# Performance work log

Measured on AMD Instinct MI355X. Metric: run time of the kernel, lower is better.

The kernel has to match this reference:

```python
import jax, jax.numpy as jnp
import numpy as np

B, N, K, DIM = 2, 20000, 16, 256


def _mlp(x, W, b):
    # torch nn.Linear: x @ W.T + b, then LeakyReLU(0.1)
    return jax.nn.leaky_relu(x @ W.T + b, negative_slope=0.1)


def _lfa(features, geom, idx, W, b):
    # features: [B, N, C]; geom: [B, N, K, 4]; idx: [B, N, K]
    t = _mlp(geom, W, b)                                  # [B, N, K, d_lfa]
    fn = jax.vmap(lambda f, i: f[i])(features, idx)       # gather neighbors: [B, N, K, C]
    # mean over K of concat == concat of means (faithful, avoids big concat)
    return jnp.concatenate([t.mean(axis=2), fn.mean(axis=2)], axis=-1)


def _linear_init(key, out_f, in_f):
    k1, k2 = jax.random.split(key)
    bound = 1.0 / np.sqrt(in_f)
    W = jax.random.uniform(k1, (out_f, in_f), jnp.float32, -bound, bound)
    b = jax.random.uniform(k2, (out_f,), jnp.float32, -bound, bound)
    return W, b


def setup_inputs() -> dict:
    key = jax.random.key(0)
    ks = jax.random.split(key, 8)
    W_init, b_init = _linear_init(ks[0], DIM // 4, DIM)
    W_l1, b_l1 = _linear_init(ks[1], DIM // 4, 4)
    W_l2, b_l2 = _linear_init(ks[2], DIM // 2, 4)
    W_fin, b_fin = _linear_init(ks[3], DIM, DIM)
    W_id, b_id = _linear_init(ks[4], DIM, DIM)
    return {
        "input_tensor": jax.random.normal(ks[5], (B, N, DIM), jnp.float32),
        "geometric_features": jax.random.normal(ks[6], (B, N, K, 4), jnp.float32),
        "neighbor_indices": jax.random.randint(ks[7], (B, N, K), 0, N, jnp.int64 if jax.config.jax_enable_x64 else jnp.int32),
        "W_init": W_init, "b_init": b_init,
        "W_l1": W_l1, "b_l1": b_l1,
        "W_l2": W_l2, "b_l2": b_l2,
        "W_fin": W_fin, "b_fin": b_fin,
        "W_id": W_id, "b_id": b_id,
    }


def reference(input_tensor, geometric_features, neighbor_indices,
              W_init, b_init, W_l1, b_l1, W_l2, b_l2,
              W_fin, b_fin, W_id, b_id):
    residual = input_tensor
    x = _mlp(input_tensor, W_init, b_init)                       # [B, N, dim/4]
    x = _lfa(x, geometric_features, neighbor_indices, W_l1, b_l1)  # [B, N, dim/2]
    x = _lfa(x, geometric_features, neighbor_indices, W_l2, b_l2)  # [B, N, dim]
    x = _mlp(x, W_fin, b_fin)
    return x + _mlp(residual, W_id, b_id)
```

## Files before the change

### kernel.cpp

```cpp
#include <hip/hip_runtime.h>
#include <hip/hip_bf16.h>

#define BN   40000
#define NPTS 20000
#define KNN  16
#define DIM  256

typedef __attribute__((ext_vector_type(8))) short bf16x8;
typedef __attribute__((ext_vector_type(4))) float f32x4;

__device__ __forceinline__ float lrelu(float v) { return v > 0.f ? v : 0.1f * v; }
__device__ __forceinline__ float bs2f(short s) {
    union { unsigned u; float f; } c; c.u = ((unsigned)(unsigned short)s) << 16;
    return c.f;
}
__device__ __forceinline__ short f2bs(float f) {
    __hip_bfloat16 h = __float2bfloat16(f);
    return *reinterpret_cast<short*>(&h);
}
__device__ __forceinline__ bf16x8 ldf32_bf16x8(const float* p) {
    const float4 a = ((const float4*)p)[0];
    const float4 b = ((const float4*)p)[1];
    bf16x8 r;
    r[0]=f2bs(a.x); r[1]=f2bs(a.y); r[2]=f2bs(a.z); r[3]=f2bs(a.w);
    r[4]=f2bs(b.x); r[5]=f2bs(b.y); r[6]=f2bs(b.z); r[7]=f2bs(b.w);
    return r;
}

__device__ __forceinline__ void dma16(const void* g, void* l) {
    __builtin_amdgcn_global_load_lds(
        (const __attribute__((address_space(1))) unsigned int*)g,
        (__attribute__((address_space(3))) unsigned int*)l, 16, 0, 0);
}

__global__ void __launch_bounds__(256) geom_kernel(
    const float* __restrict__ geom,
    const float* __restrict__ W1, const float* __restrict__ B1,
    const float* __restrict__ W2, const float* __restrict__ B2,
    const int* __restrict__ idxw, int* __restrict__ flag,
    const float* __restrict__ Wf, const float* __restrict__ Wi,
    const float* __restrict__ Wn,
    short* __restrict__ Wt, short* __restrict__ Wnt,
    __hip_bfloat16* __restrict__ x2,
    __hip_bfloat16* __restrict__ x3)
{
    if (blockIdx.x >= 3751) {
        int t = (blockIdx.x - 3751) * 256 + threadIdx.x;
        if (t < 32768) {
            int mat = (t >> 14) & 1;
            int tt  = t & 16383;
            float4 v = mat ? ((const float4*)Wi)[tt] : ((const float4*)Wf)[tt];
            int n  = tt >> 6;
            int k  = (tt & 63) * 4;
            int kk = k >> 5, q = (k >> 3) & 3, j = k & 7;
            short4 o; o.x=f2bs(v.x); o.y=f2bs(v.y); o.z=f2bs(v.z); o.w=f2bs(v.w);
            *(short4*)(Wt + ((size_t)((kk*2 + mat)*4 + q))*2048 + n*8 + j) = o;
        } else {
            int tt = t - 32768;
            float4 v = ((const float4*)Wn)[tt];
            int n  = tt >> 6;
            int k  = (tt & 63) * 4;
            int kk = k >> 5, q = (k >> 3) & 3, j = k & 7;
            short4 o; o.x=f2bs(v.x); o.y=f2bs(v.y); o.z=f2bs(v.z); o.w=f2bs(v.w);
            *(short4*)(Wnt + ((size_t)((kk*4 + q)*64 + n))*8 + j) = o;
        }
        return;
    }
    if (blockIdx.x == 3750) {
        __shared__ int red[256];
        int t = threadIdx.x;
        int v = 0;
#pragma unroll
        for (int it = 0; it < 64; ++it)
            v |= idxw[2 * (t + it * 256) + 1];
        red[t] = v;
        __syncthreads();
        for (int s = 128; s > 0; s >>= 1) {
            if (t < s) red[t] |= red[t + s];
            __syncthreads();
        }
        if (t == 0) *flag = (red[0] != 0) ? 1 : 0;
        return;
    }
    int tid = blockIdx.x * 256 + threadIdx.x;
    int p  = tid / 24;
    int cg = tid - p * 24;
    const float4* g = (const float4*)(geom + (size_t)p * (KNN * 4));
    const float4* Wp; const float* Bp; int c0;
    if (cg < 8) { c0 = cg * 8;       Wp = (const float4*)W1; Bp = B1; }
    else        { c0 = (cg - 8) * 8; Wp = (const float4*)W2; Bp = B2; }
    float4 w[8]; float bb[8];
#pragma unroll
    for (int j = 0; j < 8; ++j) { w[j] = Wp[c0 + j]; bb[j] = Bp[c0 + j]; }
    float acc[8];
#pragma unroll
    for (int j = 0; j < 8; ++j) acc[j] = 0.f;
#pragma unroll
    for (int k = 0; k < KNN; ++k) {
        float4 gv = g[k];
#pragma unroll
        for (int j = 0; j < 8; ++j)
            acc[j] += lrelu(bb[j] + gv.x*w[j].x + gv.y*w[j].y + gv.z*w[j].z + gv.w*w[j].w);
    }
    const float s = 1.f/16.f;
    short* dst = (cg < 8) ? ((short*)x2 + (size_t)p*128 + c0)
                          : ((short*)x3 + (size_t)p*256 + c0);
    bf16x8 o;
#pragma unroll
    for (int j = 0; j < 8; ++j) o[j] = f2bs(acc[j] * s);
    *(bf16x8*)dst = o;
}

__global__ void __launch_bounds__(256) mlp_init_mfma(
    const float* __restrict__ X,
    const short* __restrict__ Wnt,
    const float* __restrict__ bias,
    __hip_bfloat16* __restrict__ Y)
{
    __shared__ short wbuf[16384];
    int t = threadIdx.x;
    int wave = t >> 6, lane = t & 63;
    int r = lane & 15, q = lane >> 4;
    {
        const char* W8 = (const char*)Wnt;
        char* L8 = (char*)wbuf;
#pragma unroll
        for (int rd = 0; rd < 8; ++rd) {
            int off = (wave * 8 + rd) * 1024 + lane * 16;
            dma16(W8 + off, L8 + off);
        }
    }
    int m0 = blockIdx.x * 64 + wave * 16;
    const float* Xs = X + (size_t)(m0 + r) * DIM + q * 8;
    bf16x8 a[8];
#pragma unroll
    for (int kk = 0; kk < 8; ++kk) a[kk] = ldf32_bf16x8(Xs + kk * 32);
    __syncthreads();

    f32x4 acc[4];
#pragma unroll
    for (int nt = 0; nt < 4; ++nt) acc[nt] = (f32x4){0.f,0.f,0.f,0.f};
#pragma unroll
    for (int kk = 0; kk < 8; ++kk) {
#pragma unroll
        for (int nt = 0; nt < 4; ++nt) {
            bf16x8 b = *(const bf16x8*)&wbuf[((kk*4 + q)*64 + nt*16 + r) * 8];
            acc[nt] = __builtin_amdgcn_mfma_f32_16x16x32_bf16(a[kk], b, acc[nt], 0, 0, 0);
        }
    }
#pragma unroll
    for (int nt = 0; nt < 4; ++nt) {
        int col = nt * 16 + r;
        float bv = bias[col];
#pragma unroll
        for (int i = 0; i < 4; ++i) {
            float v = lrelu(acc[nt][i] + bv);
            Y[(size_t)(m0 + q*4 + i) * 64 + col] = __float2bfloat16(v);
        }
    }
}

__global__ void __launch_bounds__(256) gather1_kernel(
    const int* __restrict__ idxw, const int* __restrict__ flag,
    const __hip_bfloat16* __restrict__ x1,
    __hip_bfloat16* __restrict__ x2)
{
    int t = blockIdx.x * 256 + threadIdx.x;
    int p = t >> 3, j = t & 7;
    int lane = threadIdx.x & 63;
    int dual = (*flag == 0) ? 2 : 1;
    int base = (p >= NPTS) ? NPTS : 0;
    int i0 = idxw[((size_t)p * 16 + 2*j)     * dual];
    int i1 = idxw[((size_t)p * 16 + 2*j + 1) * dual];
    int g8 = lane & 56;
    float acc[8];
#pragma unroll
    for (int i = 0; i < 8; ++i) acc[i] = 0.f;
#pragma unroll
    for (int k = 0; k < 8; ++k) {
        int rA = base + __shfl(i0, g8 + k, 64);
        int rB = base + __shfl(i1, g8 + k, 64);
        bf16x8 vA = *(const bf16x8*)((const short*)x1 + (size_t)rA * 64 + j * 8);
        bf16x8 vB = *(const bf16x8*)((const short*)x1 + (size_t)rB * 64 + j * 8);
#pragma unroll
        for (int i = 0; i < 8; ++i) acc[i] += bs2f(vA[i]) + bs2f(vB[i]);
    }
    bf16x8 o;
#pragma unroll
    for (int i = 0; i < 8; ++i) o[i] = f2bs(acc[i] * (1.f/16.f));
    *(bf16x8*)((short*)x2 + (size_t)p * 128 + 64 + j * 8) = o;
}

__global__ void __launch_bounds__(256) gather2_kernel(
    const int* __restrict__ idxw, const int* __restrict__ flag,
    const __hip_bfloat16* __restrict__ x2,
    __hip_bfloat16* __restrict__ x3)
{
    int t = blockIdx.x * 256 + threadIdx.x;
    int p = t >> 4, j = t & 15;
    int lane = threadIdx.x & 63;
    int dual = (*flag == 0) ? 2 : 1;
    int base = (p >= NPTS) ? NPTS : 0;
    int myi = idxw[((size_t)p * 16 + j) * dual];
    int g16 = lane & 48;
    float acc[8];
#pragma unroll
    for (int i = 0; i < 8; ++i) acc[i] = 0.f;
#pragma unroll
    for (int k = 0; k < KNN; ++k) {
        int row = base + __shfl(myi, g16 + k, 64);
        bf16x8 v = *(const bf16x8*)((const short*)x2 + (size_t)row * 128 + j * 8);
#pragma unroll
        for (int i = 0; i < 8; ++i) acc[i] += bs2f(v[i]);
    }
    bf16x8 o;
#pragma unroll
    for (int i = 0; i < 8; ++i) o[i] = f2bs(acc[i] * (1.f/16.f));
    *(bf16x8*)((short*)x3 + (size_t)p * 256 + 128 + j * 8) = o;
}

__global__ void __launch_bounds__(512, 2) final_mfma(
    const __hip_bfloat16* __restrict__ X3,
    const float* __restrict__ RES,
    const short* __restrict__ Wt,
    const float* __restrict__ Bf,
    const float* __restrict__ Bi,
    float* __restrict__ OUT)
{
    __shared__ short lw[65536];
    const int t    = threadIdx.x;
    const int wave = t >> 6, lane = t & 63;
    const int r = lane & 15, q = lane >> 4;
    const int rg = wave >> 1, cg = wave & 1;
    const int ch = blockIdx.x & 1;
    const int p0 = (blockIdx.x >> 1) * 320;

    {
        const char* WtB = (const char*)Wt;
        char* L = (char*)lw;
#pragma unroll
        for (int i = 0; i < 16; ++i) {
            int c = wave * 8 + (i >> 1);
            int d = i & 1;
            int mat = c >> 5, kk = (c >> 2) & 7, qq = c & 3;
            int src_sh = ((kk * 2 + mat) * 4 + qq) * 2048 + ch * 1024;
            dma16(WtB + (size_t)src_sh * 2 + d * 1024 + lane * 16,
                  L + (c * 2 + d) * 1024 + lane * 16);
        }
    }
    const int cb = ch * 128 + cg * 64;
    float bfv[4], biv[4];
#pragma unroll
    for (int nt = 0; nt < 4; ++nt) {
        bfv[nt] = Bf[cb + nt * 16 + r];
        biv[nt] = Bi[cb + nt * 16 + r];
    }
    __syncthreads();

    const short* bpf = lw + q * 1024 + (cg * 64 + r) * 8;
    const short* bpi = bpf + 32768;

#pragma unroll
    for (int tt = 0; tt < 5; ++tt) {
        const int row = p0 + tt * 64 + rg * 16 + r;
        const short* x3r = (const short*)X3 + (size_t)row * DIM + q * 8;
        const float* rsr = RES + (size_t)row * DIM + q * 8;

        bf16x8 a1[8];
        float4 rw[16];
#pragma unroll
        for (int kk = 0; kk < 8; ++kk) {
            rw[2*kk]   = ((const float4*)rsr)[kk * 8];
            rw[2*kk+1] = ((const float4*)rsr)[kk * 8 + 1];
            a1[kk] = *(const bf16x8*)(x3r + kk * 32);
        }

        f32x4 acc1[4], acc2[4];
#pragma unroll
        for (int nt = 0; nt < 4; ++nt) {
            acc1[nt] = (f32x4){0.f,0.f,0.f,0.f};
            acc2[nt] = (f32x4){0.f,0.f,0.f,0.f};
        }
#pragma unroll
        for (int kk = 0; kk < 8; ++kk) {
            bf16x8 a2;
            {
                const float4 lo = rw[2*kk], hi = rw[2*kk+1];
                a2[0]=f2bs(lo.x); a2[1]=f2bs(lo.y); a2[2]=f2bs(lo.z); a2[3]=f2bs(lo.w);
                a2[4]=f2bs(hi.x); a2[5]=f2bs(hi.y); a2[6]=f2bs(hi.z); a2[7]=f2bs(hi.w);
            }
#pragma unroll
            for (int nt = 0; nt < 4; ++nt) {
                bf16x8 b1 = *(const bf16x8*)(bpf + kk * 4096 + nt * 128);
                bf16x8 b2 = *(const bf16x8*)(bpi + kk * 4096 + nt * 128);
                acc1[nt] = __builtin_amdgcn_mfma_f32_16x16x32_bf16(a1[kk], b1, acc1[nt], 0, 0, 0);
                acc2[nt] = __builtin_amdgcn_mfma_f32_16x16x32_bf16(a2,    b2, acc2[nt], 0, 0, 0);
            }
        }
#pragma unroll
        for (int nt = 0; nt < 4; ++nt) {
            const int col = cb + nt * 16 + r;
#pragma unroll
            for (int i = 0; i < 4; ++i) {
                float v = lrelu(acc1[nt][i] + bfv[nt]) + lrelu(acc2[nt][i] + biv[nt]);
                OUT[(size_t)(p0 + tt * 64 + rg * 16 + q * 4 + i) * DIM + col] = v;
            }
        }
    }
}

extern "C" void kernel_launch(void* const* d_in, const int* in_sizes, int n_in,
                              void* d_out, int out_size, void* d_ws, size_t ws_size,
                              hipStream_t stream)
{
    const float* input  = (const float*)d_in[0];
    const float* geom   = (const float*)d_in[1];
    const int*   idxw   = (const int*)d_in[2];
    const float* W_init = (const float*)d_in[3];
    const float* b_init = (const float*)d_in[4];
    const float* W_l1   = (const float*)d_in[5];
    const float* b_l1   = (const float*)d_in[6];
    const float* W_l2   = (const float*)d_in[7];
    const float* b_l2   = (const float*)d_in[8];
    const float* W_fin  = (const float*)d_in[9];
    const float* b_fin  = (const float*)d_in[10];
    const float* W_id   = (const float*)d_in[11];
    const float* b_id   = (const float*)d_in[12];
    float* out = (float*)d_out;

    char* ws = (char*)d_ws;
    int* flag = (int*)ws;
    short* Wt  = (short*)(ws + 16);
    short* Wnt = (short*)(ws + 16 + 262144);
    __hip_bfloat16* x2 = (__hip_bfloat16*)(ws + 16 + 5120000);
    __hip_bfloat16* x3 = (__hip_bfloat16*)(ws + 16 + 15360000);
    __hip_bfloat16* x1 = (__hip_bfloat16*)d_out;

    geom_kernel<<<3895, 256, 0, stream>>>(geom, W_l1, b_l1, W_l2, b_l2,
                                          idxw, flag, W_fin, W_id, W_init,
                                          Wt, Wnt, x2, x3);
    mlp_init_mfma<<<625, 256, 0, stream>>>(input, Wnt, b_init, x1);
    gather1_kernel<<<1250, 256, 0, stream>>>(idxw, flag, x1, x2);
    gather2_kernel<<<2500, 256, 0, stream>>>(idxw, flag, x2, x3);
    final_mfma<<<250, 512, 0, stream>>>(x3, input, Wt, b_fin, b_id, out);
}
```

Measured before the change: 208.1 us.

## Compute geometric MLP with 32x32x16 bf16 MFMA instead of scalar FMAs

The per-point geometric-feature MLP (4 inputs to 64 and 128 outputs, averaged over 16 neighbors) is recast as matrix-core work. Each wave handles two points: 32 neighbor rows by 4 features, zero-padded to K=16, multiplied against six 32-column weight tiles with mfma_f32_32x32x16_bf16. The neighbor mean is then a register reduction plus a cross-half shuffle. LeakyReLU becomes a branchless fmax. Inputs and weights are rounded to bf16 before the matmul, which lowers precision, and most of each MFMA's K dimension is padding.

```diff
diff --git a/kernel.cpp b/kernel.cpp
--- a/kernel.cpp
+++ b/kernel.cpp
@@ -8,8 +8,9 @@
 
 typedef __attribute__((ext_vector_type(8))) short bf16x8;
 typedef __attribute__((ext_vector_type(4))) float f32x4;
-
-__device__ __forceinline__ float lrelu(float v) { return v > 0.f ? v : 0.1f * v; }
+typedef __attribute__((ext_vector_type(16))) float f32x16;
+
+__device__ __forceinline__ float lrelu(float v) { return fmaxf(v, 0.1f * v); }
 __device__ __forceinline__ float bs2f(short s) {
     union { unsigned u; float f; } c; c.u = ((unsigned)(unsigned short)s) << 16;
     return c.f;
@@ -44,8 +45,8 @@
     __hip_bfloat16* __restrict__ x2,
     __hip_bfloat16* __restrict__ x3)
 {
-    if (blockIdx.x >= 3751) {
-        int t = (blockIdx.x - 3751) * 256 + threadIdx.x;
+    if (blockIdx.x >= 5001) {
+        int t = (blockIdx.x - 5001) * 256 + threadIdx.x;
         if (t < 32768) {
             int mat = (t >> 14) & 1;
             int tt  = t & 16383;
@@ -66,7 +67,7 @@
         }
         return;
     }
-    if (blockIdx.x == 3750) {
+    if (blockIdx.x == 5000) {
         __shared__ int red[256];
         int t = threadIdx.x;
         int v = 0;
@@ -82,33 +83,52 @@
         if (t == 0) *flag = (red[0] != 0) ? 1 : 0;
         return;
     }
-    int tid = blockIdx.x * 256 + threadIdx.x;
-    int p  = tid / 24;
-    int cg = tid - p * 24;
-    const float4* g = (const float4*)(geom + (size_t)p * (KNN * 4));
-    const float4* Wp; const float* Bp; int c0;
-    if (cg < 8) { c0 = cg * 8;       Wp = (const float4*)W1; Bp = B1; }
-    else        { c0 = (cg - 8) * 8; Wp = (const float4*)W2; Bp = B2; }
-    float4 w[8]; float bb[8];
-#pragma unroll
-    for (int j = 0; j < 8; ++j) { w[j] = Wp[c0 + j]; bb[j] = Bp[c0 + j]; }
-    float acc[8];
-#pragma unroll
-    for (int j = 0; j < 8; ++j) acc[j] = 0.f;
-#pragma unroll
-    for (int k = 0; k < KNN; ++k) {
-        float4 gv = g[k];
-#pragma unroll
-        for (int j = 0; j < 8; ++j)
-            acc[j] += lrelu(bb[j] + gv.x*w[j].x + gv.y*w[j].y + gv.z*w[j].z + gv.w*w[j].w);
-    }
-    const float s = 1.f/16.f;
-    short* dst = (cg < 8) ? ((short*)x2 + (size_t)p*128 + c0)
-                          : ((short*)x3 + (size_t)p*256 + c0);
-    bf16x8 o;
-#pragma unroll
-    for (int j = 0; j < 8; ++j) o[j] = f2bs(acc[j] * s);
-    *(bf16x8*)dst = o;
+    const int lane = threadIdx.x & 63;
+    const int wv   = threadIdx.x >> 6;
+    const int p0   = (blockIdx.x * 4 + wv) * 2;
+    const int c31  = lane & 31;
+    const int hi   = lane >> 5;
+
+    bf16x8 a = (bf16x8){0,0,0,0,0,0,0,0};
+    if (hi == 0) {
+        const float4 g = *(const float4*)(
+            geom + ((size_t)(p0 + (c31 >> 4)) * KNN + (c31 & 15)) * 4);
+        a[0]=f2bs(g.x); a[1]=f2bs(g.y); a[2]=f2bs(g.z); a[3]=f2bs(g.w);
+    }
+    bf16x8 bfr[6]; float bv[6];
+#pragma unroll
+    for (int tt = 0; tt < 6; ++tt) {
+        bfr[tt] = (bf16x8){0,0,0,0,0,0,0,0};
+        const float* Wrow;
+        if (tt < 2) { Wrow = W1 + (size_t)(tt*32 + c31) * 4;     bv[tt] = B1[tt*32 + c31]; }
+        else        { Wrow = W2 + (size_t)((tt-2)*32 + c31) * 4; bv[tt] = B2[(tt-2)*32 + c31]; }
+        if (hi == 0) {
+            const float4 w4 = *(const float4*)Wrow;
+            bfr[tt][0]=f2bs(w4.x); bfr[tt][1]=f2bs(w4.y);
+            bfr[tt][2]=f2bs(w4.z); bfr[tt][3]=f2bs(w4.w);
+        }
+    }
+    f32x16 acc[6];
+#pragma unroll
+    for (int tt = 0; tt < 6; ++tt) {
+#pragma unroll
+        for (int i = 0; i < 16; ++i) acc[tt][i] = 0.f;
+        acc[tt] = __builtin_amdgcn_mfma_f32_32x32x16_bf16(a, bfr[tt], acc[tt], 0, 0, 0);
+    }
+#pragma unroll
+    for (int tt = 0; tt < 6; ++tt) {
+        float sA = 0.f, sB = 0.f;
+#pragma unroll
+        for (int i = 0; i < 8; ++i)  sA += lrelu(acc[tt][i]     + bv[tt]);
+#pragma unroll
+        for (int i = 0; i < 8; ++i)  sB += lrelu(acc[tt][i + 8] + bv[tt]);
+        sA += __shfl_xor(sA, 32, 64);
+        sB += __shfl_xor(sB, 32, 64);
+        const float s = (hi ? sB : sA) * (1.f / 16.f);
+        const short v = f2bs(s);
+        if (tt < 2) ((short*)x2)[(size_t)(p0 + hi) * 128 + tt*32 + c31] = v;
+        else        ((short*)x3)[(size_t)(p0 + hi) * 256 + (tt-2)*32 + c31] = v;
+    }
 }
 
 __global__ void __launch_bounds__(256) mlp_init_mfma(
@@ -151,10 +171,10 @@
 #pragma unroll
     for (int nt = 0; nt < 4; ++nt) {
         int col = nt * 16 + r;
-        float bv = bias[col];
+        float bvx = bias[col];
 #pragma unroll
         for (int i = 0; i < 4; ++i) {
-            float v = lrelu(acc[nt][i] + bv);
+            float v = lrelu(acc[nt][i] + bvx);
             Y[(size_t)(m0 + q*4 + i) * 64 + col] = __float2bfloat16(v);
         }
     }
@@ -336,7 +356,7 @@
     __hip_bfloat16* x3 = (__hip_bfloat16*)(ws + 16 + 15360000);
     __hip_bfloat16* x1 = (__hip_bfloat16*)d_out;
 
-    geom_kernel<<<3895, 256, 0, stream>>>(geom, W_l1, b_l1, W_l2, b_l2,
+    geom_kernel<<<5145, 256, 0, stream>>>(geom, W_l1, b_l1, W_l2, b_l2,
                                           idxw, flag, W_fin, W_id, W_init,
                                           Wt, Wnt, x2, x3);
     mlp_init_mfma<<<625, 256, 0, stream>>>(input, Wnt, b_init, x1);
```

Measured after the change: 206.4 us. No clear change (-0.8%).
